# Performance work log

Measured on AMD Instinct MI355X. Metric: run time of the kernel, lower is better.

Reference implementation:

```python
import jax, jax.numpy as jnp
import numpy as np

T, K, E, D, F = 2048, 6, 32, 2048, 1408   # tokens, top_k, routed experts, dim, moe_inter_dim
S = 2                                      # fused shared experts
C = T * K // E                             # exact per-expert capacity (balanced routing)


def _silu_and_mul(gu):
    # merged gate_up activation: silu(gate_half) * up_half
    g, u = jnp.split(gu, 2, axis=-1)
    return jax.nn.silu(g) * u


def setup_inputs() -> dict:
    key = jax.random.key(0)
    ks = jax.random.split(key, 7)
    x = jax.random.normal(ks[0], (T, D), dtype=jnp.float32)
    # balanced routing: every expert receives exactly C = T*K/E token-expert pairs
    indices = jax.random.permutation(ks[1], jnp.arange(T * K, dtype=jnp.int32) % E).reshape(T, K)
    weights = jax.random.uniform(ks[2], (T, K), dtype=jnp.float32)
    scale = 0.02
    w_gate_up = jax.random.normal(ks[3], (E, D, 2 * F), dtype=jnp.float32) * scale
    w_down = jax.random.normal(ks[4], (E, F, D), dtype=jnp.float32) * scale
    w_gate_up_shared = jax.random.normal(ks[5], (S, D, 2 * F), dtype=jnp.float32) * scale
    w_down_shared = jax.random.normal(ks[6], (S, F, D), dtype=jnp.float32) * scale
    return {"x": x, "weights": weights, "w_gate_up": w_gate_up, "w_down": w_down,
            "w_gate_up_shared": w_gate_up_shared, "w_down_shared": w_down_shared,
            "indices": indices}


def reference(x, weights, w_gate_up, w_down, w_gate_up_shared, w_down_shared, indices):
    # ---- dispatch: sort token-expert pairs by expert id (balanced -> exactly C per expert)
    flat_e = indices.reshape(-1)                       # [T*K]
    order = jnp.argsort(flat_e, stable=True)           # [T*K] pair ids grouped by expert
    tok = order // K                                   # source token of each sorted pair
    w_sorted = weights.reshape(-1)[order]              # routing weight of each sorted pair
    xg = x[tok].reshape(E, C, D)                       # gathered per-expert inputs
    # ---- routed experts: grouped gate_up GEMM -> silu_and_mul -> down GEMM
    act = _silu_and_mul(jnp.einsum('ecd,edf->ecf', xg, w_gate_up))   # [E, C, F]
    down = jnp.einsum('ecf,efd->ecd', act, w_down)                   # [E, C, D]
    # ---- combine: weighted scatter-add back to token order (y[idx] += out * weights[idx, top])
    y = jnp.zeros_like(x).at[tok].add(down.reshape(E * C, D) * w_sorted[:, None])
    # ---- fused shared experts: run on all tokens, added unweighted
    act_s = _silu_and_mul(jnp.einsum('td,sdf->stf', x, w_gate_up_shared))  # [S, T, F]
    y = y + jnp.einsum('stf,sfd->td', act_s, w_down_shared)
    return y
```

## Files before the change

### kernel.cpp

```cpp
#include <hip/hip_runtime.h>
#include <hip/hip_bf16.h>

#define TT 2048
#define KK 6
#define EE 32
#define DD 2048
#define FF 1408
#define SS 2
#define CC 384

typedef __bf16 bf16_t;
typedef __attribute__((ext_vector_type(8))) __bf16 bf16x8;
typedef __attribute__((ext_vector_type(4))) float f32x4;
typedef unsigned int u32;

#define AS1 __attribute__((address_space(1)))
#define AS3 __attribute__((address_space(3)))

__device__ __forceinline__ u32 f2bf(float f) {
    u32 u = __builtin_bit_cast(u32, f);
    return (u + 0x7fffu + ((u >> 16) & 1u)) >> 16;
}
__device__ __forceinline__ u32 pack2(float a, float b) {
    return f2bf(a) | (f2bf(b) << 16);
}

__global__ void k_dispatch(const int* __restrict__ idx, int* __restrict__ counts,
                           int* __restrict__ tok, int* __restrict__ sop) {
    int p = blockIdx.x * 256 + threadIdx.x;
    if (p >= TT * KK) return;
    int e = idx[p];
    int pos = atomicAdd(&counts[e], 1);
    int slot = e * CC + pos;
    tok[slot] = p / KK;
    sop[p] = slot;
}

__global__ void k_gather(const float* __restrict__ x, const int* __restrict__ tok,
                         bf16_t* __restrict__ xall) {
    int row = blockIdx.x;
    int srow = (row < EE * CC) ? tok[row] : (row - EE * CC);
    const float* src = x + (size_t)srow * DD;
    bf16_t* dst = xall + (size_t)row * DD;
    int c0 = threadIdx.x * 8;
    float4 a = *(const float4*)(src + c0);
    float4 b = *(const float4*)(src + c0 + 4);
    uint4 o;
    o.x = pack2(a.x, a.y); o.y = pack2(a.z, a.w);
    o.z = pack2(b.x, b.y); o.w = pack2(b.z, b.w);
    *(uint4*)(dst + c0) = o;
}

#define BSTR 40

__global__ __launch_bounds__(256) void k_gemm_r(
    const bf16_t* __restrict__ Aall, const float* __restrict__ Br,
    bf16_t* __restrict__ Out, int Kdim, int N)
{
    const int e = blockIdx.y;
    const int n0 = blockIdx.x * 64;
    const bf16_t* A = Aall + (size_t)e * CC * Kdim;
    const float* Bp = Br + (size_t)e * Kdim * N + n0;
    bf16_t* Cout = Out + (size_t)e * CC * N + n0;

    __shared__ __align__(16) bf16_t As[CC * 32];
    __shared__ __align__(16) bf16_t Bs[64 * BSTR];

    const int tid = threadIdx.x;
    const int lane = tid & 63, wid = tid >> 6;
    const int m_base = wid * 96;
    const int l15 = lane & 15, lq = lane >> 4;

    f32x4 acc[6][4] = {};

    const int arow = tid >> 2;
    const int ac   = tid & 3;
    const int bn = tid & 63, kb = (tid >> 6) * 8;

    const int ksteps = Kdim >> 5;
    for (int kt = 0; kt < ksteps; ++kt) {
        const int k0 = kt << 5;
        #pragma unroll
        for (int i = 0; i < 6; ++i) {
            const int row = i * 64 + arow;
            const int cs = ac ^ (row & 3);
            const bf16_t* g = A + (size_t)row * Kdim + (k0 + cs * 8);
            AS3 u32* l = (AS3 u32*)(void*)(As + (size_t)(i * 64 + wid * 16) * 32);
            __builtin_amdgcn_global_load_lds((const AS1 u32*)(const void*)g, l, 16, 0, 0);
        }
        {
            const float* bg = Bp + (size_t)(k0 + kb) * N + bn;
            float v[8];
            #pragma unroll
            for (int j = 0; j < 8; ++j) v[j] = bg[(size_t)j * N];
            uint4 w;
            w.x = pack2(v[0], v[1]); w.y = pack2(v[2], v[3]);
            w.z = pack2(v[4], v[5]); w.w = pack2(v[6], v[7]);
            *(uint4*)(Bs + (size_t)bn * BSTR + kb) = w;
        }
        __syncthreads();
        bf16x8 bfr[4];
        #pragma unroll
        for (int j = 0; j < 4; ++j)
            bfr[j] = *(const bf16x8*)(Bs + (size_t)(j * 16 + l15) * BSTR + lq * 8);
        #pragma unroll
        for (int m = 0; m < 6; ++m) {
            const int row = m_base + m * 16 + l15;
            bf16x8 af = *(const bf16x8*)(As + (size_t)row * 32 + (size_t)((lq ^ (row & 3)) * 8));
            #pragma unroll
            for (int j = 0; j < 4; ++j)
                acc[m][j] = __builtin_amdgcn_mfma_f32_16x16x32_bf16(af, bfr[j], acc[m][j], 0, 0, 0);
        }
        __syncthreads();
    }

    #pragma unroll
    for (int m = 0; m < 6; ++m) {
        #pragma unroll
        for (int j = 0; j < 4; ++j) {
            const int n = j * 16 + l15;
            #pragma unroll
            for (int r = 0; r < 4; ++r) {
                const int mm = m_base + m * 16 + lq * 4 + r;
                Cout[(size_t)mm * N + n] = (bf16_t)acc[m][j][r];
            }
        }
    }
}

__global__ __launch_bounds__(256) void k_gemm_s(
    const bf16_t* __restrict__ Ash, const float* __restrict__ Bsh,
    bf16_t* __restrict__ Out, int Kdim, int N, int ash_stride)
{
    const int s = blockIdx.z;
    const bf16_t* A = Ash + ((size_t)s * ash_stride + (size_t)blockIdx.y * 128) * Kdim;
    bf16_t* Cout = Out + ((size_t)s * TT + (size_t)blockIdx.y * 128) * N + (size_t)blockIdx.x * 128;
    const float* Bp = Bsh + (size_t)s * Kdim * N + (size_t)blockIdx.x * 128;

    __shared__ __align__(16) bf16_t As[128 * 32];
    __shared__ __align__(16) bf16_t Bs[128 * BSTR];

    const int tid = threadIdx.x;
    const int lane = tid & 63, wid = tid >> 6;
    const int m_off = (wid >> 1) * 64, n_off = (wid & 1) * 64;
    const int l15 = lane & 15, lq = lane >> 4;

    f32x4 acc[4][4] = {};

    const int arow = tid >> 2;
    const int ac   = tid & 3;
    const int bn = tid & 127, kb = (tid >> 7) * 16;

    const int ksteps = Kdim >> 5;
    for (int kt = 0; kt < ksteps; ++kt) {
        const int k0 = kt << 5;
        {
            const int cs = ac ^ (arow & 3);
            const bf16_t* g0 = A + (size_t)arow * Kdim + (k0 + cs * 8);
            const bf16_t* g1 = A + (size_t)(arow + 64) * Kdim + (k0 + cs * 8);
            AS3 u32* l0 = (AS3 u32*)(void*)(As + (size_t)(wid * 16) * 32);
            AS3 u32* l1 = (AS3 u32*)(void*)(As + (size_t)(64 + wid * 16) * 32);
            __builtin_amdgcn_global_load_lds((const AS1 u32*)(const void*)g0, l0, 16, 0, 0);
            __builtin_amdgcn_global_load_lds((const AS1 u32*)(const void*)g1, l1, 16, 0, 0);
        }
        {
            const float* bg = Bp + (size_t)(k0 + kb) * N + bn;
            float v[16];
            #pragma unroll
            for (int j = 0; j < 16; ++j) v[j] = bg[(size_t)j * N];
            u32 p[8];
            #pragma unroll
            for (int j = 0; j < 8; ++j) p[j] = pack2(v[2 * j], v[2 * j + 1]);
            uint4 w0, w1;
            w0.x = p[0]; w0.y = p[1]; w0.z = p[2]; w0.w = p[3];
            w1.x = p[4]; w1.y = p[5]; w1.z = p[6]; w1.w = p[7];
            *(uint4*)(Bs + (size_t)bn * BSTR + kb) = w0;
            *(uint4*)(Bs + (size_t)bn * BSTR + kb + 8) = w1;
        }
        __syncthreads();
        bf16x8 af[4], bfr[4];
        #pragma unroll
        for (int i = 0; i < 4; ++i) {
            const int row = m_off + i * 16 + l15;
            af[i] = *(const bf16x8*)(As + (size_t)row * 32 + (size_t)((lq ^ (row & 3)) * 8));
        }
        #pragma unroll
        for (int j = 0; j < 4; ++j)
            bfr[j] = *(const bf16x8*)(Bs + (size_t)(n_off + j * 16 + l15) * BSTR + lq * 8);
        #pragma unroll
        for (int i = 0; i < 4; ++i)
            #pragma unroll
            for (int j = 0; j < 4; ++j)
                acc[i][j] = __builtin_amdgcn_mfma_f32_16x16x32_bf16(af[i], bfr[j], acc[i][j], 0, 0, 0);
        __syncthreads();
    }

    #pragma unroll
    for (int i = 0; i < 4; ++i) {
        #pragma unroll
        for (int j = 0; j < 4; ++j) {
            int n = n_off + j * 16 + l15;
            #pragma unroll
            for (int r = 0; r < 4; ++r) {
                int m = m_off + i * 16 + lq * 4 + r;
                Cout[(size_t)m * N + n] = (bf16_t)acc[i][j][r];
            }
        }
    }
}

__global__ void k_silu(const bf16_t* __restrict__ gu, bf16_t* __restrict__ act) {
    u32 f = ((u32)blockIdx.x * 256 + threadIdx.x) * 8;
    u32 row = f / FF;
    u32 col = f % FF;
    const bf16_t* base = gu + (size_t)row * (2 * FF) + col;
    bf16x8 g = *(const bf16x8*)(base);
    bf16x8 u = *(const bf16x8*)(base + FF);
    bf16x8 ov;
    #pragma unroll
    for (int j = 0; j < 8; ++j) {
        float gf = (float)g[j], uf = (float)u[j];
        float s = gf / (1.0f + __expf(-gf));
        ov[j] = (bf16_t)(s * uf);
    }
    *(bf16x8*)(act + (size_t)row * FF + col) = ov;
}

__global__ void k_combine(const bf16_t* __restrict__ down, const int* __restrict__ sop,
                          const float* __restrict__ wts, float* __restrict__ y) {
    int t = blockIdx.x;
    int d0 = threadIdx.x * 8;
    float a[8] = {0, 0, 0, 0, 0, 0, 0, 0};
    #pragma unroll
    for (int k = 0; k < KK; ++k) {
        int slot = sop[t * KK + k];
        float w = wts[t * KK + k];
        bf16x8 v = *(const bf16x8*)(down + (size_t)slot * DD + d0);
        #pragma unroll
        for (int j = 0; j < 8; ++j) a[j] += w * (float)v[j];
    }
    #pragma unroll
    for (int s = 0; s < SS; ++s) {
        bf16x8 v = *(const bf16x8*)(down + ((size_t)EE * CC + (size_t)s * TT + t) * DD + d0);
        #pragma unroll
        for (int j = 0; j < 8; ++j) a[j] += (float)v[j];
    }
    float4 o0, o1;
    o0.x = a[0]; o0.y = a[1]; o0.z = a[2]; o0.w = a[3];
    o1.x = a[4]; o1.y = a[5]; o1.z = a[6]; o1.w = a[7];
    *(float4*)(y + (size_t)t * DD + d0) = o0;
    *(float4*)(y + (size_t)t * DD + d0 + 4) = o1;
}

extern "C" void kernel_launch(void* const* d_in, const int* in_sizes, int n_in,
                              void* d_out, int out_size, void* d_ws, size_t ws_size,
                              hipStream_t stream) {
    (void)in_sizes; (void)n_in; (void)out_size; (void)ws_size;
    const float* x      = (const float*)d_in[0];
    const float* wts    = (const float*)d_in[1];
    const float* w_gu   = (const float*)d_in[2];
    const float* w_dn   = (const float*)d_in[3];
    const float* w_gu_s = (const float*)d_in[4];
    const float* w_dn_s = (const float*)d_in[5];
    const int*   indices= (const int*)d_in[6];
    float* y = (float*)d_out;

    char* ws = (char*)d_ws;
    size_t off = 0;
    auto alloc = [&](size_t bytes) {
        void* p = ws + off;
        off = (off + bytes + 255) & ~(size_t)255;
        return p;
    };
    int*    counts = (int*)alloc((size_t)EE * 4);
    int*    tok    = (int*)alloc((size_t)EE * CC * 4);
    int*    sop    = (int*)alloc((size_t)TT * KK * 4);
    bf16_t* xall   = (bf16_t*)alloc((size_t)(EE * CC + TT) * DD * 2);
    bf16_t* gu     = (bf16_t*)alloc((size_t)(EE * CC + SS * TT) * 2 * FF * 2);
    bf16_t* actb   = (bf16_t*)alloc((size_t)(EE * CC + SS * TT) * FF * 2);
    bf16_t* dnout  = (bf16_t*)alloc((size_t)(EE * CC + SS * TT) * DD * 2);

    hipMemsetAsync(counts, 0, EE * 4, stream);
    k_dispatch<<<(TT * KK + 255) / 256, 256, 0, stream>>>(indices, counts, tok, sop);
    k_gather<<<EE * CC + TT, 256, 0, stream>>>(x, tok, xall);

    k_gemm_r<<<dim3(2 * FF / 64, EE), 256, 0, stream>>>(xall, w_gu, gu, DD, 2 * FF);
    k_gemm_s<<<dim3(2 * FF / 128, TT / 128, SS), 256, 0, stream>>>(
        xall + (size_t)EE * CC * DD, w_gu_s, gu + (size_t)EE * CC * 2 * FF, DD, 2 * FF, 0);

    k_silu<<<(EE * CC + SS * TT) * FF / 8 / 256, 256, 0, stream>>>(gu, actb);

    k_gemm_r<<<dim3(DD / 64, EE), 256, 0, stream>>>(actb, w_dn, dnout, FF, DD);
    k_gemm_s<<<dim3(DD / 128, TT / 128, SS), 256, 0, stream>>>(
        actb + (size_t)EE * CC * FF, w_dn_s, dnout + (size_t)EE * CC * DD, FF, DD, TT);

    k_combine<<<TT, 256, 0, stream>>>(dnout, sop, wts, y);
}
```

Before: 1.783 ms.

## Double-buffer LDS tiles in routed and shared expert GEMMs to overlap loads

Both GEMM kernels now hold two LDS buffers for the A and B tiles. The next k-step's A tile is issued by direct global-to-LDS loads and its B values are loaded into registers before the current step's MFMAs run. The B values are converted to bf16 and written to the other buffer afterwards, so one barrier per k-step is removed and global latency can hide behind compute. The cost is twice the shared memory (about 55 KB for k_gemm_r), which can lower occupancy, plus extra registers for the prefetched values.

```diff
diff --git a/kernel.cpp b/kernel.cpp
--- a/kernel.cpp
+++ b/kernel.cpp
@@ -53,6 +53,18 @@
 
 #define BSTR 40
 
+__device__ __forceinline__ void stage_a6(const bf16_t* __restrict__ A, int Kdim, int k0,
+                                         bf16_t* dst, int arow, int ac, int wid) {
+    #pragma unroll
+    for (int i = 0; i < 6; ++i) {
+        const int row = i * 64 + arow;
+        const int cs = ac ^ (row & 3);
+        const bf16_t* g = A + (size_t)row * Kdim + (k0 + cs * 8);
+        AS3 u32* l = (AS3 u32*)(void*)(dst + (size_t)(i * 64 + wid * 16) * 32);
+        __builtin_amdgcn_global_load_lds((const AS1 u32*)(const void*)g, l, 16, 0, 0);
+    }
+}
+
 __global__ __launch_bounds__(256) void k_gemm_r(
     const bf16_t* __restrict__ Aall, const float* __restrict__ Br,
     bf16_t* __restrict__ Out, int Kdim, int N)
@@ -63,8 +75,8 @@
     const float* Bp = Br + (size_t)e * Kdim * N + n0;
     bf16_t* Cout = Out + (size_t)e * CC * N + n0;
 
-    __shared__ __align__(16) bf16_t As[CC * 32];
-    __shared__ __align__(16) bf16_t Bs[64 * BSTR];
+    __shared__ __align__(16) bf16_t As[2][CC * 32];
+    __shared__ __align__(16) bf16_t Bs[2][64 * BSTR];
 
     const int tid = threadIdx.x;
     const int lane = tid & 63, wid = tid >> 6;
@@ -78,40 +90,51 @@
     const int bn = tid & 63, kb = (tid >> 6) * 8;
 
     const int ksteps = Kdim >> 5;
+
+    {
+        stage_a6(A, Kdim, 0, &As[0][0], arow, ac, wid);
+        const float* bg = Bp + (size_t)kb * N + bn;
+        float v[8];
+        #pragma unroll
+        for (int j = 0; j < 8; ++j) v[j] = bg[(size_t)j * N];
+        uint4 w;
+        w.x = pack2(v[0], v[1]); w.y = pack2(v[2], v[3]);
+        w.z = pack2(v[4], v[5]); w.w = pack2(v[6], v[7]);
+        *(uint4*)(&Bs[0][0] + (size_t)bn * BSTR + kb) = w;
+    }
+    __syncthreads();
+
+    int cur = 0;
     for (int kt = 0; kt < ksteps; ++kt) {
-        const int k0 = kt << 5;
-        #pragma unroll
-        for (int i = 0; i < 6; ++i) {
-            const int row = i * 64 + arow;
-            const int cs = ac ^ (row & 3);
-            const bf16_t* g = A + (size_t)row * Kdim + (k0 + cs * 8);
-            AS3 u32* l = (AS3 u32*)(void*)(As + (size_t)(i * 64 + wid * 16) * 32);
-            __builtin_amdgcn_global_load_lds((const AS1 u32*)(const void*)g, l, 16, 0, 0);
-        }
-        {
-            const float* bg = Bp + (size_t)(k0 + kb) * N + bn;
-            float v[8];
-            #pragma unroll
-            for (int j = 0; j < 8; ++j) v[j] = bg[(size_t)j * N];
-            uint4 w;
-            w.x = pack2(v[0], v[1]); w.y = pack2(v[2], v[3]);
-            w.z = pack2(v[4], v[5]); w.w = pack2(v[6], v[7]);
-            *(uint4*)(Bs + (size_t)bn * BSTR + kb) = w;
-        }
-        __syncthreads();
+        const bool pf = (kt + 1 < ksteps);
+        float vn[8];
+        if (pf) {
+            const int k1 = (kt + 1) << 5;
+            stage_a6(A, Kdim, k1, &As[cur ^ 1][0], arow, ac, wid);
+            const float* bg = Bp + (size_t)(k1 + kb) * N + bn;
+            #pragma unroll
+            for (int j = 0; j < 8; ++j) vn[j] = bg[(size_t)j * N];
+        }
         bf16x8 bfr[4];
         #pragma unroll
         for (int j = 0; j < 4; ++j)
-            bfr[j] = *(const bf16x8*)(Bs + (size_t)(j * 16 + l15) * BSTR + lq * 8);
+            bfr[j] = *(const bf16x8*)(&Bs[cur][0] + (size_t)(j * 16 + l15) * BSTR + lq * 8);
         #pragma unroll
         for (int m = 0; m < 6; ++m) {
             const int row = m_base + m * 16 + l15;
-            bf16x8 af = *(const bf16x8*)(As + (size_t)row * 32 + (size_t)((lq ^ (row & 3)) * 8));
+            bf16x8 af = *(const bf16x8*)(&As[cur][0] + (size_t)row * 32 + (size_t)((lq ^ (row & 3)) * 8));
             #pragma unroll
             for (int j = 0; j < 4; ++j)
                 acc[m][j] = __builtin_amdgcn_mfma_f32_16x16x32_bf16(af, bfr[j], acc[m][j], 0, 0, 0);
         }
+        if (pf) {
+            uint4 w;
+            w.x = pack2(vn[0], vn[1]); w.y = pack2(vn[2], vn[3]);
+            w.z = pack2(vn[4], vn[5]); w.w = pack2(vn[6], vn[7]);
+            *(uint4*)(&Bs[cur ^ 1][0] + (size_t)bn * BSTR + kb) = w;
+        }
         __syncthreads();
+        cur ^= 1;
     }
 
     #pragma unroll
@@ -137,8 +160,8 @@
     bf16_t* Cout = Out + ((size_t)s * TT + (size_t)blockIdx.y * 128) * N + (size_t)blockIdx.x * 128;
     const float* Bp = Bsh + (size_t)s * Kdim * N + (size_t)blockIdx.x * 128;
 
-    __shared__ __align__(16) bf16_t As[128 * 32];
-    __shared__ __align__(16) bf16_t Bs[128 * BSTR];
+    __shared__ __align__(16) bf16_t As[2][128 * 32];
+    __shared__ __align__(16) bf16_t Bs[2][128 * BSTR];
 
     const int tid = threadIdx.x;
     const int lane = tid & 63, wid = tid >> 6;
@@ -152,47 +175,71 @@
     const int bn = tid & 127, kb = (tid >> 7) * 16;
 
     const int ksteps = Kdim >> 5;
+
+    auto stageA = [&](int b, int k0) {
+        const int cs = ac ^ (arow & 3);
+        const bf16_t* g0 = A + (size_t)arow * Kdim + (k0 + cs * 8);
+        const bf16_t* g1 = A + (size_t)(arow + 64) * Kdim + (k0 + cs * 8);
+        AS3 u32* l0 = (AS3 u32*)(void*)(&As[b][0] + (size_t)(wid * 16) * 32);
+        AS3 u32* l1 = (AS3 u32*)(void*)(&As[b][0] + (size_t)(64 + wid * 16) * 32);
+        __builtin_amdgcn_global_load_lds((const AS1 u32*)(const void*)g0, l0, 16, 0, 0);
+        __builtin_amdgcn_global_load_lds((const AS1 u32*)(const void*)g1, l1, 16, 0, 0);
+    };
+
+    {
+        stageA(0, 0);
+        const float* bg = Bp + (size_t)kb * N + bn;
+        float v[16];
+        #pragma unroll
+        for (int j = 0; j < 16; ++j) v[j] = bg[(size_t)j * N];
+        u32 p[8];
+        #pragma unroll
+        for (int j = 0; j < 8; ++j) p[j] = pack2(v[2 * j], v[2 * j + 1]);
+        uint4 w0, w1;
+        w0.x = p[0]; w0.y = p[1]; w0.z = p[2]; w0.w = p[3];
+        w1.x = p[4]; w1.y = p[5]; w1.z = p[6]; w1.w = p[7];
+        *(uint4*)(&Bs[0][0] + (size_t)bn * BSTR + kb) = w0;
+        *(uint4*)(&Bs[0][0] + (size_t)bn * BSTR + kb + 8) = w1;
+    }
+    __syncthreads();
+
+    int cur = 0;
     for (int kt = 0; kt < ksteps; ++kt) {
-        const int k0 = kt << 5;
-        {
-            const int cs = ac ^ (arow & 3);
-            const bf16_t* g0 = A + (size_t)arow * Kdim + (k0 + cs * 8);
-            const bf16_t* g1 = A + (size_t)(arow + 64) * Kdim + (k0 + cs * 8);
-            AS3 u32* l0 = (AS3 u32*)(void*)(As + (size_t)(wid * 16) * 32);
-            AS3 u32* l1 = (AS3 u32*)(void*)(As + (size_t)(64 + wid * 16) * 32);
-            __builtin_amdgcn_global_load_lds((const AS1 u32*)(const void*)g0, l0, 16, 0, 0);
-            __builtin_amdgcn_global_load_lds((const AS1 u32*)(const void*)g1, l1, 16, 0, 0);
-        }
-        {
-            const float* bg = Bp + (size_t)(k0 + kb) * N + bn;
-            float v[16];
-            #pragma unroll
-            for (int j = 0; j < 16; ++j) v[j] = bg[(size_t)j * N];
+        const bool pf = (kt + 1 < ksteps);
+        float vn[16];
+        if (pf) {
+            const int k1 = (kt + 1) << 5;
+            stageA(cur ^ 1, k1);
+            const float* bg = Bp + (size_t)(k1 + kb) * N + bn;
+            #pragma unroll
+            for (int j = 0; j < 16; ++j) vn[j] = bg[(size_t)j * N];
+        }
+        bf16x8 af[4], bfr[4];
+        #pragma unroll
+        for (int i = 0; i < 4; ++i) {
+            const int row = m_off + i * 16 + l15;
+            af[i] = *(const bf16x8*)(&As[cur][0] + (size_t)row * 32 + (size_t)((lq ^ (row & 3)) * 8));
+        }
+        #pragma unroll
+        for (int j = 0; j < 4; ++j)
+            bfr[j] = *(const bf16x8*)(&Bs[cur][0] + (size_t)(n_off + j * 16 + l15) * BSTR + lq * 8);
+        #pragma unroll
+        for (int i = 0; i < 4; ++i)
+            #pragma unroll
+            for (int j = 0; j < 4; ++j)
+                acc[i][j] = __builtin_amdgcn_mfma_f32_16x16x32_bf16(af[i], bfr[j], acc[i][j], 0, 0, 0);
+        if (pf) {
             u32 p[8];
             #pragma unroll
-            for (int j = 0; j < 8; ++j) p[j] = pack2(v[2 * j], v[2 * j + 1]);
+            for (int j = 0; j < 8; ++j) p[j] = pack2(vn[2 * j], vn[2 * j + 1]);
             uint4 w0, w1;
             w0.x = p[0]; w0.y = p[1]; w0.z = p[2]; w0.w = p[3];
             w1.x = p[4]; w1.y = p[5]; w1.z = p[6]; w1.w = p[7];
-            *(uint4*)(Bs + (size_t)bn * BSTR + kb) = w0;
-            *(uint4*)(Bs + (size_t)bn * BSTR + kb + 8) = w1;
+            *(uint4*)(&Bs[cur ^ 1][0] + (size_t)bn * BSTR + kb) = w0;
+            *(uint4*)(&Bs[cur ^ 1][0] + (size_t)bn * BSTR + kb + 8) = w1;
         }
         __syncthreads();
-        bf16x8 af[4], bfr[4];
-        #pragma unroll
-        for (int i = 0; i < 4; ++i) {
-            const int row = m_off + i * 16 + l15;
-            af[i] = *(const bf16x8*)(As + (size_t)row * 32 + (size_t)((lq ^ (row & 3)) * 8));
-        }
-        #pragma unroll
-        for (int j = 0; j < 4; ++j)
-            bfr[j] = *(const bf16x8*)(Bs + (size_t)(n_off + j * 16 + l15) * BSTR + lq * 8);
-        #pragma unroll
-        for (int i = 0; i < 4; ++i)
-            #pragma unroll
-            for (int j = 0; j < 4; ++j)
-                acc[i][j] = __builtin_amdgcn_mfma_f32_16x16x32_bf16(af[i], bfr[j], acc[i][j], 0, 0, 0);
-        __syncthreads();
+        cur ^= 1;
     }
 
     #pragma unroll
```

New measurement: 1.614 ms. 1.1x faster.
